# Kernel tuning notes

Measured on AMD Instinct MI355X. Metric: run time of the kernel, lower is better.

## Reference

```python
import jax, jax.numpy as jnp
import numpy as np

N = 512      # nodes
E = 16384    # edges (avg degree 32)
D = 128      # indim
OUT = 128    # outdim


def setup_inputs() -> dict:
    key = jax.random.key(0)
    k1, k2, k3 = jax.random.split(key, 3)
    X = jax.random.normal(k1, (N, N, D), dtype=jnp.float32)
    edge_index = jax.random.randint(k2, (2, E), 0, N, dtype=jnp.int64)
    W = jax.random.normal(k3, (3 * D, OUT), dtype=jnp.float32) * (1.0 / np.sqrt(3 * D))
    b = jnp.zeros((OUT,), dtype=jnp.float32)
    return {"X": X, "edge_index": edge_index, "W": W, "b": b}


def reference(X, edge_index, W, b):
    # X: [N, N, D] tuple features X[i, j] for (subgraph root i, node j)
    # edge_index: [2, E] directed edges (src -> dst), aggr = 'sum'
    n = X.shape[0]
    src, dst = edge_index[0], edge_index[1]
    # Dense binary adjacency (sum aggregation counts multi-edges, matching
    # scatter-add over the edge list). A[k, j] = #edges k -> j.
    A = jnp.zeros((n, n), dtype=X.dtype).at[src, dst].add(jnp.ones((src.shape[0],), X.dtype))
    # OpMessagePassingOnSubg2D: within subgraph i, aggregate over neighbors of j
    # X1[i, j] = sum_{k in N(j)} X[i, k]
    X1 = jnp.einsum('kj,ikd->ijd', A, X)
    # OpMessagePassingCrossSubg2D: across subgraphs, aggregate over neighbors of i
    # X2[i, j] = sum_{k in N(i)} X[k, j]
    X2 = jnp.einsum('ki,kjd->ijd', A, X)
    # catvalue([X1, X2]) -> [X, X1, X2], then pointwise MLP (single Linear)
    H = jnp.concatenate([X, X1, X2], axis=-1)  # [N, N, 3D]
    return H @ W + b  # [N, N, OUT]
```

## Files before the change

kernel.cpp:

```cpp
#include <hip/hip_runtime.h>
#include <hip/hip_bf16.h>
#include <stdint.h>

#define NN 512
#define DD 128
#define EE 16384
#define K3 384

typedef short bf16x8 __attribute__((ext_vector_type(8)));
typedef short bf16x4 __attribute__((ext_vector_type(4)));
typedef float f32x4  __attribute__((ext_vector_type(4)));

__device__ __forceinline__ short f2bf(float f) {
    union { __hip_bfloat16 h; short s; } u;
    u.h = __float2bfloat16(f);
    return u.s;
}

typedef __attribute__((address_space(3))) unsigned int lds_u32;
typedef __attribute__((address_space(1))) const unsigned int glb_u32;
__device__ __forceinline__ void gll16(void* l, const void* g) {
    __builtin_amdgcn_global_load_lds((glb_u32*)g, (lds_u32*)l, 16, 0, 0);
}


__global__ void k_zero(float* __restrict__ At) {
    At[blockIdx.x * 256 + threadIdx.x] = 0.0f;
}

__global__ void k_edges(const int* __restrict__ ei, float* __restrict__ At) {
    __shared__ int flag;
    if (threadIdx.x == 0) flag = 0;
    __syncthreads();
    int any = 0;
    for (int i = threadIdx.x; i < EE; i += blockDim.x) any |= ei[2 * i + 1];
    if (any) atomicOr(&flag, 1);
    __syncthreads();
    const bool is32 = (flag != 0);
    for (int e = threadIdx.x; e < EE; e += blockDim.x) {
        int src, dst;
        if (is32) { src = ei[e];     dst = ei[EE + e]; }
        else      { src = ei[2 * e]; dst = ei[2 * (EE + e)]; }
        atomicAdd(&At[dst * NN + src], 1.0f);
    }
}

__global__ void k_cast_at(const float* __restrict__ At, short* __restrict__ Atb) {
    int t = blockIdx.x * 256 + threadIdx.x;
    Atb[t] = f2bf(At[t]);
}

__global__ void k_wt(const float* __restrict__ W, short* __restrict__ Wt) {
    int t = blockIdx.x * 256 + threadIdx.x;
    int kk = t >> 7, n = t & 127;
    Wt[n * K3 + kk] = f2bf(W[t]);
}

__global__ __launch_bounds__(256) void k_prep(const float* __restrict__ X,
                                              short* __restrict__ XbT,
                                              short* __restrict__ XT2) {
    __shared__ __align__(16) short T[128 * 128];
    const int tid = threadIdx.x;
    const int b = blockIdx.x;
    int sbase, rstride, dbase;
    short* dst;
    if (b < 2048) {
        int i = b >> 2, k0 = (b & 3) * 128;
        sbase = i * 65536 + k0 * 128; rstride = 128;
        dbase = i * 65536 + k0; dst = XbT;
    } else {
        int bb = b - 2048;
        int j = bb >> 2, i0 = (bb & 3) * 128;
        sbase = i0 * 65536 + j * 128; rstride = 65536;
        dbase = j * 65536 + i0; dst = XT2;
    }
    #pragma unroll
    for (int it = 0; it < 16; ++it) {
        int g = tid + it * 256;
        int r = g >> 5, c4 = (g & 31) * 4;
        float4 v = *(const float4*)&X[sbase + r * rstride + c4];
        bf16x4 p; p[0] = f2bf(v.x); p[1] = f2bf(v.y); p[2] = f2bf(v.z); p[3] = f2bf(v.w);
        int cs = c4 ^ (((r >> 3) & 7) << 2);
        *(bf16x4*)&T[r * 128 + cs] = p;
    }
    __syncthreads();
    #pragma unroll
    for (int it = 0; it < 8; ++it) {
        int q = tid + it * 256;
        int d = q >> 4, ck = (q & 15) * 8;
        bf16x8 p;
        #pragma unroll
        for (int j = 0; j < 8; ++j) {
            int k = ck + j;
            p[j] = T[k * 128 + (d ^ (((k >> 3) & 7) << 2))];
        }
        *(bf16x8*)&dst[dbase + d * 512 + ck] = p;
    }
}

__global__ __launch_bounds__(256) void k_aggg(const short* __restrict__ Atb,
                                              const short* __restrict__ Bsrc,
                                              short* __restrict__ C,
                                              int mode) {
    __shared__ __align__(16) short sm[16384];
    short* As = sm;
    short* Bs = sm + 8192;

    const int tid  = threadIdx.x;
    const int lane = tid & 63;
    const int wv   = tid >> 6;
    const int wr   = (wv >> 1) * 64;
    const int wc   = (wv & 1) * 64;
    const int lm   = lane & 15;
    const int lq   = lane >> 4;

    const int inst = blockIdx.x >> 2, t4 = blockIdx.x & 3;
    const int a0 = t4 * 128;
    const int Bbase = inst * 65536;
    int Cbase, Crs;
    if (mode == 0) { Cbase = inst * 65536 + t4 * 16384; Crs = 128; }
    else           { Cbase = t4 * 8388608 + inst * 128; Crs = 65536; }

    int srow[4], scg[4];
    #pragma unroll
    for (int it = 0; it < 4; ++it) {
        int s = it * 256 + tid;
        int r = s >> 3, p = s & 7;
        srow[it] = r; scg[it] = (p ^ (r & 7)) * 8;
    }

    f32x4 acc[4][4] = {};

    for (int kb = 0; kb < 8; ++kb) {
        const int k0 = kb * 64;
        #pragma unroll
        for (int it = 0; it < 4; ++it) {
            int slot = it * 256 + tid;
            gll16(&As[slot * 8], &Atb[(a0 + srow[it]) * 512 + k0 + scg[it]]);
            gll16(&Bs[slot * 8], &Bsrc[Bbase + srow[it] * 512 + k0 + scg[it]]);
        }
        __syncthreads();
        #pragma unroll
        for (int ks = 0; ks < 2; ++ks) {
            bf16x8 af[4], bf[4];
            #pragma unroll
            for (int mf = 0; mf < 4; ++mf) {
                int R = wr + mf * 16 + lm, Cc = ks * 4 + lq;
                af[mf] = *(const bf16x8*)&As[R * 64 + (Cc ^ (R & 7)) * 8];
            }
            #pragma unroll
            for (int nf = 0; nf < 4; ++nf) {
                int R = wc + nf * 16 + lm, Cc = ks * 4 + lq;
                bf[nf] = *(const bf16x8*)&Bs[R * 64 + (Cc ^ (R & 7)) * 8];
            }
            #pragma unroll
            for (int mf = 0; mf < 4; ++mf)
                #pragma unroll
                for (int nf = 0; nf < 4; ++nf)
                    acc[mf][nf] = __builtin_amdgcn_mfma_f32_16x16x32_bf16(
                        af[mf], bf[nf], acc[mf][nf], 0, 0, 0);
        }
        __syncthreads();
    }

    #pragma unroll
    for (int mf = 0; mf < 4; ++mf)
        #pragma unroll
        for (int nf = 0; nf < 4; ++nf)
            #pragma unroll
            for (int r = 0; r < 4; ++r)
                sm[(wr + mf * 16 + lq * 4 + r) * 128 + wc + nf * 16 + lm]
                    = f2bf(acc[mf][nf][r]);
    __syncthreads();
    #pragma unroll
    for (int it = 0; it < 8; ++it) {
        int q = tid + it * 256;
        int orow = q >> 4, oc = (q & 15) * 8;
        *(bf16x8*)&C[Cbase + orow * Crs + oc] = *(const bf16x8*)&sm[orow * 128 + oc];
    }
}

__global__ __launch_bounds__(256) void k_final2(const float* __restrict__ X,
                                                const short* __restrict__ X1b,
                                                const short* __restrict__ X2b,
                                                const short* __restrict__ Wt,
                                                const float* __restrict__ bias,
                                                float* __restrict__ out) {
    __shared__ __align__(16) short sm[16384];
    short* As = sm;
    short* Ws = sm + 8192;

    const int tid  = threadIdx.x;
    const int lane = tid & 63;
    const int wv   = tid >> 6;
    const int wr   = (wv >> 1) * 64;
    const int wc   = (wv & 1) * 64;
    const int lm   = lane & 15;
    const int lq   = lane >> 4;
    const int m0   = blockIdx.x * 128;

    int srow[4], scg[4];
    #pragma unroll
    for (int it = 0; it < 4; ++it) {
        int s = it * 256 + tid;
        int r = s >> 3, p = s & 7;
        srow[it] = r; scg[it] = (p ^ (r & 7)) * 8;
    }

    f32x4 acc[4][4] = {};

    for (int ph = 0; ph < 6; ++ph) {
        const int s = ph >> 1, h = ph & 1;
        const int kw0 = s * 128 + h * 64;
        if (s == 0) {
            #pragma unroll
            for (int it = 0; it < 4; ++it) {
                int slot = it * 256 + tid;
                const float* xp = &X[(m0 + srow[it]) * 128 + h * 64 + scg[it]];
                float4 v0 = *(const float4*)xp;
                float4 v1 = *(const float4*)(xp + 4);
                bf16x8 pk;
                pk[0] = f2bf(v0.x); pk[1] = f2bf(v0.y); pk[2] = f2bf(v0.z); pk[3] = f2bf(v0.w);
                pk[4] = f2bf(v1.x); pk[5] = f2bf(v1.y); pk[6] = f2bf(v1.z); pk[7] = f2bf(v1.w);
                *(bf16x8*)&As[slot * 8] = pk;
            }
        } else {
            const short* src = (s == 1) ? X1b : X2b;
            #pragma unroll
            for (int it = 0; it < 4; ++it)
                gll16(&As[(it * 256 + tid) * 8],
                      &src[(m0 + srow[it]) * 128 + h * 64 + scg[it]]);
        }
        #pragma unroll
        for (int it = 0; it < 4; ++it)
            gll16(&Ws[(it * 256 + tid) * 8],
                  &Wt[srow[it] * K3 + kw0 + scg[it]]);
        __syncthreads();
        #pragma unroll
        for (int ks = 0; ks < 2; ++ks) {
            bf16x8 af[4], bf[4];
            #pragma unroll
            for (int mf = 0; mf < 4; ++mf) {
                int R = wr + mf * 16 + lm, Cc = ks * 4 + lq;
                af[mf] = *(const bf16x8*)&As[R * 64 + (Cc ^ (R & 7)) * 8];
            }
            #pragma unroll
            for (int nf = 0; nf < 4; ++nf) {
                int R = wc + nf * 16 + lm, Cc = ks * 4 + lq;
                bf[nf] = *(const bf16x8*)&Ws[R * 64 + (Cc ^ (R & 7)) * 8];
            }
            #pragma unroll
            for (int mf = 0; mf < 4; ++mf)
                #pragma unroll
                for (int nf = 0; nf < 4; ++nf)
                    acc[mf][nf] = __builtin_amdgcn_mfma_f32_16x16x32_bf16(
                        af[mf], bf[nf], acc[mf][nf], 0, 0, 0);
        }
        __syncthreads();
    }

    #pragma unroll
    for (int nf = 0; nf < 4; ++nf) {
        float bv = bias[wc + nf * 16 + lm];
        #pragma unroll
        for (int mf = 0; mf < 4; ++mf)
            #pragma unroll
            for (int r = 0; r < 4; ++r) {
                int row = m0 + wr + mf * 16 + lq * 4 + r;
                int col = wc + nf * 16 + lm;
                out[row * 128 + col] = acc[mf][nf][r] + bv;
            }
    }
}


__global__ __launch_bounds__(256) void k_agg_fb(const float* __restrict__ X,
                                                const float* __restrict__ At,
                                                short* __restrict__ X1b,
                                                short* __restrict__ X2b) {
    __shared__ short As[128 * 72];
    __shared__ short Bs[128 * 72];
    const int tid  = threadIdx.x;
    const int lane = tid & 63;
    const int wv   = tid >> 6;
    const int wr   = (wv >> 1) * 64;
    const int wc   = (wv & 1) * 64;
    const int lm   = lane & 15;
    const int lq   = lane >> 4;
    int a0, Bbase, Bks, Cbase, Crs;
    short* Cp;
    const int bidx = blockIdx.x;
    if (bidx < 2048) {
        int i = bidx >> 2, jt = bidx & 3;
        a0 = jt * 128; Bbase = i * 65536; Bks = 128;
        Cbase = i * 65536 + jt * 16384; Crs = 128; Cp = X1b;
    } else {
        int bb = bidx - 2048;
        int j = bb >> 2, it = bb & 3;
        a0 = it * 128; Bbase = j * 128; Bks = 65536;
        Cbase = it * 8388608 + j * 128; Crs = 65536; Cp = X2b;
    }
    f32x4 acc[4][4] = {};
    const int d  = tid & 127;
    const int kh = tid >> 7;
    for (int kb = 0; kb < 8; ++kb) {
        const int k0 = kb * 64;
        #pragma unroll
        for (int it8 = 0; it8 < 8; ++it8) {
            int g = tid + it8 * 256;
            int r = g >> 4, kq = (g & 15) * 4;
            float4 v = *(const float4*)&At[(a0 + r) * 512 + k0 + kq];
            bf16x4 p; p[0] = f2bf(v.x); p[1] = f2bf(v.y); p[2] = f2bf(v.z); p[3] = f2bf(v.w);
            *(bf16x4*)&As[r * 72 + kq] = p;
        }
        #pragma unroll
        for (int gi = 0; gi < 4; ++gi) {
            int kg = kh * 4 + gi;
            bf16x8 p;
            #pragma unroll
            for (int j = 0; j < 8; ++j)
                p[j] = f2bf(X[Bbase + (k0 + kg * 8 + j) * Bks + d]);
            *(bf16x8*)&Bs[d * 72 + kg * 8] = p;
        }
        __syncthreads();
        #pragma unroll
        for (int ks = 0; ks < 2; ++ks) {
            bf16x8 af[4], bfr[4];
            #pragma unroll
            for (int mf = 0; mf < 4; ++mf)
                af[mf] = *(const bf16x8*)&As[(wr + mf * 16 + lm) * 72 + ks * 32 + lq * 8];
            #pragma unroll
            for (int nf = 0; nf < 4; ++nf)
                bfr[nf] = *(const bf16x8*)&Bs[(wc + nf * 16 + lm) * 72 + ks * 32 + lq * 8];
            #pragma unroll
            for (int mf = 0; mf < 4; ++mf)
                #pragma unroll
                for (int nf = 0; nf < 4; ++nf)
                    acc[mf][nf] = __builtin_amdgcn_mfma_f32_16x16x32_bf16(
                        af[mf], bfr[nf], acc[mf][nf], 0, 0, 0);
        }
        __syncthreads();
    }
    #pragma unroll
    for (int mf = 0; mf < 4; ++mf)
        #pragma unroll
        for (int nf = 0; nf < 4; ++nf)
            #pragma unroll
            for (int r = 0; r < 4; ++r) {
                int row = wr + mf * 16 + lq * 4 + r;
                int col = wc + nf * 16 + lm;
                Cp[Cbase + row * Crs + col] = f2bf(acc[mf][nf][r]);
            }
}

__global__ __launch_bounds__(256) void k_final_fb(const float* __restrict__ X,
                                                  const short* __restrict__ X1b,
                                                  const short* __restrict__ X2b,
                                                  const short* __restrict__ Wt,
                                                  const float* __restrict__ bias,
                                                  float* __restrict__ out) {
    __shared__ short As[128 * 72];
    __shared__ short Ws[128 * 72];
    const int tid  = threadIdx.x;
    const int lane = tid & 63;
    const int wv   = tid >> 6;
    const int wr   = (wv >> 1) * 64;
    const int wc   = (wv & 1) * 64;
    const int lm   = lane & 15;
    const int lq   = lane >> 4;
    const int m0   = blockIdx.x * 128;
    f32x4 acc[4][4] = {};
    for (int ph = 0; ph < 6; ++ph) {
        const int s = ph >> 1, h = ph & 1;
        if (s == 0) {
            #pragma unroll
            for (int it8 = 0; it8 < 8; ++it8) {
                int g = tid + it8 * 256;
                int r = g >> 4, kq = (g & 15) * 4;
                float4 v = *(const float4*)&X[(m0 + r) * 128 + h * 64 + kq];
                bf16x4 p; p[0] = f2bf(v.x); p[1] = f2bf(v.y); p[2] = f2bf(v.z); p[3] = f2bf(v.w);
                *(bf16x4*)&As[r * 72 + kq] = p;
            }
        } else {
            const short* src = (s == 1) ? X1b : X2b;
            #pragma unroll
            for (int it4 = 0; it4 < 4; ++it4) {
                int g = tid + it4 * 256;
                int r = g >> 3, ko = (g & 7) * 8;
                *(bf16x8*)&As[r * 72 + ko] =
                    *(const bf16x8*)&src[(m0 + r) * 128 + h * 64 + ko];
            }
        }
        #pragma unroll
        for (int it4 = 0; it4 < 4; ++it4) {
            int g = tid + it4 * 256;
            int n = g >> 3, ko = (g & 7) * 8;
            *(bf16x8*)&Ws[n * 72 + ko] =
                *(const bf16x8*)&Wt[n * K3 + s * 128 + h * 64 + ko];
        }
        __syncthreads();
        #pragma unroll
        for (int ks = 0; ks < 2; ++ks) {
            bf16x8 af[4], bfr[4];
            #pragma unroll
            for (int mf = 0; mf < 4; ++mf)
                af[mf] = *(const bf16x8*)&As[(wr + mf * 16 + lm) * 72 + ks * 32 + lq * 8];
            #pragma unroll
            for (int nf = 0; nf < 4; ++nf)
                bfr[nf] = *(const bf16x8*)&Ws[(wc + nf * 16 + lm) * 72 + ks * 32 + lq * 8];
            #pragma unroll
            for (int mf = 0; mf < 4; ++mf)
                #pragma unroll
                for (int nf = 0; nf < 4; ++nf)
                    acc[mf][nf] = __builtin_amdgcn_mfma_f32_16x16x32_bf16(
                        af[mf], bfr[nf], acc[mf][nf], 0, 0, 0);
        }
        __syncthreads();
    }
    #pragma unroll
    for (int nf = 0; nf < 4; ++nf) {
        float bv = bias[wc + nf * 16 + lm];
        #pragma unroll
        for (int mf = 0; mf < 4; ++mf)
            #pragma unroll
            for (int r = 0; r < 4; ++r) {
                int row = m0 + wr + mf * 16 + lq * 4 + r;
                int col = wc + nf * 16 + lm;
                out[row * 128 + col] = acc[mf][nf][r] + bv;
            }
    }
}

extern "C" void kernel_launch(void* const* d_in, const int* in_sizes, int n_in,
                              void* d_out, int out_size, void* d_ws, size_t ws_size,
                              hipStream_t stream) {
    const float* X  = (const float*)d_in[0];
    const int*   ei = (const int*)d_in[1];
    const float* W  = (const float*)d_in[2];
    const float* b  = (const float*)d_in[3];
    float* out = (float*)d_out;
    char* ws = (char*)d_ws;
    const size_t MB = 1u << 20;

    float* At  = (float*)ws;
    short* Atb = (short*)(ws + 1 * MB);
    short* Wt  = (short*)(ws + 1 * MB + 512 * 1024);

    k_zero <<<1024, 256, 0, stream>>>(At);
    k_edges<<<1, 1024, 0, stream>>>(ei, At);
    k_wt   <<<192, 256, 0, stream>>>(W, Wt);

    if (ws_size >= 194 * MB) {
        short* X1b = (short*)(ws + 2 * MB);
        short* XT2 = (short*)(ws + 66 * MB);
        short* XbT = (short*)(ws + 130 * MB);
        short* X2b = XbT;
        k_cast_at<<<1024, 256, 0, stream>>>(At, Atb);
        k_prep   <<<4096, 256, 0, stream>>>(X, XbT, XT2);
        k_aggg   <<<2048, 256, 0, stream>>>(Atb, XbT, X1b, 0);
        k_aggg   <<<2048, 256, 0, stream>>>(Atb, XT2, X2b, 1);
        k_final2 <<<2048, 256, 0, stream>>>(X, X1b, X2b, Wt, b, out);
    } else {
        short* X1b = (short*)(ws + 2 * MB);
        short* X2b = (short*)(ws + 66 * MB);
        k_agg_fb  <<<4096, 256, 0, stream>>>(X, At, X1b, X2b);
        k_final_fb<<<2048, 256, 0, stream>>>(X, X1b, X2b, Wt, b, out);
    }
}
```

Before: 513.5 us.

## Reassociate linear layer before aggregation: apply W slices to X then aggregate

Uses linearity to compute Y1=X·W1 and Y2=X·W2 first, then aggregates with the adjacency (A^T applied per subgraph and across subgraphs), adding X·W0, the partial and the bias in a fused final kernel. This replaces the X prep/transposes and the separate final GEMM over a 384-wide concatenation, so X is read fewer times and no X1/X2 intermediates are stored. In exchange it adds a separate transpose kernel for Y2, an extra bf16 rounding of intermediate partial sums, and some leftover dead loads in the epilogue.

```diff
diff --git a/kernel.cpp b/kernel.cpp
--- a/kernel.cpp
+++ b/kernel.cpp
@@ -10,11 +10,15 @@
 typedef short bf16x8 __attribute__((ext_vector_type(8)));
 typedef short bf16x4 __attribute__((ext_vector_type(4)));
 typedef float f32x4  __attribute__((ext_vector_type(4)));
+typedef unsigned int u32;
 
 __device__ __forceinline__ short f2bf(float f) {
     union { __hip_bfloat16 h; short s; } u;
     u.h = __float2bfloat16(f);
     return u.s;
+}
+__device__ __forceinline__ u32 pk2(float a, float b) {
+    return (u32)(unsigned short)f2bf(a) | ((u32)(unsigned short)f2bf(b) << 16);
 }
 
 typedef __attribute__((address_space(3))) unsigned int lds_u32;
@@ -50,61 +54,19 @@
     Atb[t] = f2bf(At[t]);
 }
 
-__global__ void k_wt(const float* __restrict__ W, short* __restrict__ Wt) {
+__global__ void k_wt2(const float* __restrict__ W, short* __restrict__ Wt2) {
     int t = blockIdx.x * 256 + threadIdx.x;
     int kk = t >> 7, n = t & 127;
-    Wt[n * K3 + kk] = f2bf(W[t]);
-}
-
-__global__ __launch_bounds__(256) void k_prep(const float* __restrict__ X,
-                                              short* __restrict__ XbT,
-                                              short* __restrict__ XT2) {
-    __shared__ __align__(16) short T[128 * 128];
-    const int tid = threadIdx.x;
-    const int b = blockIdx.x;
-    int sbase, rstride, dbase;
-    short* dst;
-    if (b < 2048) {
-        int i = b >> 2, k0 = (b & 3) * 128;
-        sbase = i * 65536 + k0 * 128; rstride = 128;
-        dbase = i * 65536 + k0; dst = XbT;
-    } else {
-        int bb = b - 2048;
-        int j = bb >> 2, i0 = (bb & 3) * 128;
-        sbase = i0 * 65536 + j * 128; rstride = 65536;
-        dbase = j * 65536 + i0; dst = XT2;
-    }
-    #pragma unroll
-    for (int it = 0; it < 16; ++it) {
-        int g = tid + it * 256;
-        int r = g >> 5, c4 = (g & 31) * 4;
-        float4 v = *(const float4*)&X[sbase + r * rstride + c4];
-        bf16x4 p; p[0] = f2bf(v.x); p[1] = f2bf(v.y); p[2] = f2bf(v.z); p[3] = f2bf(v.w);
-        int cs = c4 ^ (((r >> 3) & 7) << 2);
-        *(bf16x4*)&T[r * 128 + cs] = p;
-    }
-    __syncthreads();
-    #pragma unroll
-    for (int it = 0; it < 8; ++it) {
-        int q = tid + it * 256;
-        int d = q >> 4, ck = (q & 15) * 8;
-        bf16x8 p;
-        #pragma unroll
-        for (int j = 0; j < 8; ++j) {
-            int k = ck + j;
-            p[j] = T[k * 128 + (d ^ (((k >> 3) & 7) << 2))];
-        }
-        *(bf16x8*)&dst[dbase + d * 512 + ck] = p;
-    }
-}
-
-__global__ __launch_bounds__(256) void k_aggg(const short* __restrict__ Atb,
-                                              const short* __restrict__ Bsrc,
-                                              short* __restrict__ C,
-                                              int mode) {
-    __shared__ __align__(16) short sm[16384];
-    short* As = sm;
-    short* Bs = sm + 8192;
+    int s = kk >> 7, d = kk & 127;
+    Wt2[s * 16384 + n * 128 + d] = f2bf(W[t]);
+}
+
+__global__ __launch_bounds__(256) void k_y(const float* __restrict__ X,
+                                           const short* __restrict__ Wt2,
+                                           short* __restrict__ Y1T,
+                                           short* __restrict__ Y2) {
+    __shared__ __align__(16) short Xs[16384];
+    __shared__ __align__(16) short Ws[16384];
 
     const int tid  = threadIdx.x;
     const int lane = tid & 63;
@@ -113,82 +75,138 @@
     const int wc   = (wv & 1) * 64;
     const int lm   = lane & 15;
     const int lq   = lane >> 4;
-
-    const int inst = blockIdx.x >> 2, t4 = blockIdx.x & 3;
-    const int a0 = t4 * 128;
-    const int Bbase = inst * 65536;
-    int Cbase, Crs;
-    if (mode == 0) { Cbase = inst * 65536 + t4 * 16384; Crs = 128; }
-    else           { Cbase = t4 * 8388608 + inst * 128; Crs = 65536; }
-
-    int srow[4], scg[4];
+    const int i  = blockIdx.x >> 2;
+    const int j0 = (blockIdx.x & 3) * 128;
+
+    #pragma unroll
+    for (int it = 0; it < 16; ++it) {
+        int g = tid + it * 256;
+        int r = g >> 5, c4 = g & 31;
+        float4 v = *(const float4*)&X[i * 65536 + (j0 + r) * 128 + c4 * 4];
+        int kb = c4 >> 4, c = c4 & 15, p = c >> 1, h2 = c & 1;
+        bf16x4 pc; pc[0] = f2bf(v.x); pc[1] = f2bf(v.y); pc[2] = f2bf(v.z); pc[3] = f2bf(v.w);
+        *(bf16x4*)&Xs[kb * 8192 + r * 64 + ((p ^ (r & 7)) * 8 + h2 * 4)] = pc;
+    }
+
+    #pragma unroll
+    for (int s = 1; s <= 2; ++s) {
+        #pragma unroll
+        for (int it = 0; it < 8; ++it) {
+            int slot = it * 256 + tid;
+            int kb = slot >> 10, rem = slot & 1023;
+            int n = rem >> 3, pc = rem & 7;
+            gll16(&Ws[slot * 8],
+                  &Wt2[s * 16384 + n * 128 + kb * 64 + ((pc ^ (n & 7)) * 8)]);
+        }
+        __syncthreads();
+
+        f32x4 acc[4][4] = {};
+        #pragma unroll
+        for (int kb = 0; kb < 2; ++kb)
+            #pragma unroll
+            for (int ks = 0; ks < 2; ++ks) {
+                bf16x8 af[4], bf[4];
+                #pragma unroll
+                for (int mf = 0; mf < 4; ++mf) {
+                    int R = wr + mf * 16 + lm, Cc = ks * 4 + lq;
+                    af[mf] = *(const bf16x8*)&Xs[kb * 8192 + R * 64 + (Cc ^ (R & 7)) * 8];
+                }
+                #pragma unroll
+                for (int nf = 0; nf < 4; ++nf) {
+                    int R = wc + nf * 16 + lm, Cc = ks * 4 + lq;
+                    bf[nf] = *(const bf16x8*)&Ws[kb * 8192 + R * 64 + (Cc ^ (R & 7)) * 8];
+                }
+                #pragma unroll
+                for (int mf = 0; mf < 4; ++mf)
+                    #pragma unroll
+                    for (int nf = 0; nf < 4; ++nf)
+                        acc[mf][nf] = __builtin_amdgcn_mfma_f32_16x16x32_bf16(
+                            af[mf], bf[nf], acc[mf][nf], 0, 0, 0);
+            }
+        __syncthreads();
+
+        if (s == 1) {
+            u32* T = (u32*)Ws;
+            #pragma unroll
+            for (int mf = 0; mf < 4; ++mf)
+                #pragma unroll
+                for (int nf = 0; nf < 4; ++nf) {
+                    int n = wc + nf * 16 + lm;
+                    int jb = wr + mf * 16 + lq * 4;
+                    int w = jb >> 1;
+                    u32 lo = pk2(acc[mf][nf][0], acc[mf][nf][1]);
+                    u32 hi = pk2(acc[mf][nf][2], acc[mf][nf][3]);
+                    uint2 val; val.x = lo; val.y = hi;
+                    *(uint2*)&T[n * 64 + (w ^ (n & 28))] = val;
+                }
+            __syncthreads();
+            #pragma unroll
+            for (int it = 0; it < 8; ++it) {
+                int ch = tid & 15, n = (tid >> 4) + it * 16;
+                uint4 q = *(const uint4*)&T[n * 64 + ((ch * 4) ^ (n & 28))];
+                *(uint4*)&Y1T[i * 65536 + n * 512 + j0 + ch * 8] = q;
+            }
+            __syncthreads();
+        } else {
+            #pragma unroll
+            for (int mf = 0; mf < 4; ++mf)
+                #pragma unroll
+                for (int nf = 0; nf < 4; ++nf)
+                    #pragma unroll
+                    for (int r = 0; r < 4; ++r)
+                        Ws[(wr + mf * 16 + lq * 4 + r) * 128 + wc + nf * 16 + lm]
+                            = f2bf(acc[mf][nf][r]);
+            __syncthreads();
+            #pragma unroll
+            for (int it = 0; it < 8; ++it) {
+                int q = tid + it * 256;
+                int row = q >> 4, oc = (q & 15) * 8;
+                *(bf16x8*)&Y2[i * 65536 + (j0 + row) * 128 + oc]
+                    = *(const bf16x8*)&Ws[row * 128 + oc];
+            }
+        }
+    }
+}
+
+__global__ __launch_bounds__(256) void k_t(const short* __restrict__ Y2,
+                                           short* __restrict__ Y2T) {
+    __shared__ __align__(16) u32 U[128 * 64];
+    const int tid = threadIdx.x;
+    const int j  = blockIdx.x >> 2;
+    const int k0 = (blockIdx.x & 3) * 128;
+
+    const int c8 = tid & 15;
+    const int a0 = tid >> 4;
     #pragma unroll
     for (int it = 0; it < 4; ++it) {
-        int s = it * 256 + tid;
-        int r = s >> 3, p = s & 7;
-        srow[it] = r; scg[it] = (p ^ (r & 7)) * 8;
-    }
-
-    f32x4 acc[4][4] = {};
-
-    for (int kb = 0; kb < 8; ++kb) {
-        const int k0 = kb * 64;
-        #pragma unroll
-        for (int it = 0; it < 4; ++it) {
-            int slot = it * 256 + tid;
-            gll16(&As[slot * 8], &Atb[(a0 + srow[it]) * 512 + k0 + scg[it]]);
-            gll16(&Bs[slot * 8], &Bsrc[Bbase + srow[it] * 512 + k0 + scg[it]]);
-        }
-        __syncthreads();
-        #pragma unroll
-        for (int ks = 0; ks < 2; ++ks) {
-            bf16x8 af[4], bf[4];
-            #pragma unroll
-            for (int mf = 0; mf < 4; ++mf) {
-                int R = wr + mf * 16 + lm, Cc = ks * 4 + lq;
-                af[mf] = *(const bf16x8*)&As[R * 64 + (Cc ^ (R & 7)) * 8];
-            }
-            #pragma unroll
-            for (int nf = 0; nf < 4; ++nf) {
-                int R = wc + nf * 16 + lm, Cc = ks * 4 + lq;
-                bf[nf] = *(const bf16x8*)&Bs[R * 64 + (Cc ^ (R & 7)) * 8];
-            }
-            #pragma unroll
-            for (int mf = 0; mf < 4; ++mf)
-                #pragma unroll
-                for (int nf = 0; nf < 4; ++nf)
-                    acc[mf][nf] = __builtin_amdgcn_mfma_f32_16x16x32_bf16(
-                        af[mf], bf[nf], acc[mf][nf], 0, 0, 0);
-        }
-        __syncthreads();
-    }
-
-    #pragma unroll
-    for (int mf = 0; mf < 4; ++mf)
-        #pragma unroll
-        for (int nf = 0; nf < 4; ++nf)
-            #pragma unroll
-            for (int r = 0; r < 4; ++r)
-                sm[(wr + mf * 16 + lq * 4 + r) * 128 + wc + nf * 16 + lm]
-                    = f2bf(acc[mf][nf][r]);
+        int a = a0 + it * 16;
+        const short* r0 = &Y2[(size_t)(k0 + 2 * a) * 65536 + j * 128 + c8 * 8];
+        bf16x8 A0 = *(const bf16x8*)r0;
+        bf16x8 A1 = *(const bf16x8*)(r0 + 65536);
+        #pragma unroll
+        for (int cc = 0; cc < 8; ++cc) {
+            int n = c8 * 8 + cc;
+            U[n * 64 + (a ^ (n & 28))] =
+                (u32)(unsigned short)A0[cc] | ((u32)(unsigned short)A1[cc] << 16);
+        }
+    }
     __syncthreads();
+    const int ch = tid & 15;
+    const int n0 = tid >> 4;
     #pragma unroll
     for (int it = 0; it < 8; ++it) {
-        int q = tid + it * 256;
-        int orow = q >> 4, oc = (q & 15) * 8;
-        *(bf16x8*)&C[Cbase + orow * Crs + oc] = *(const bf16x8*)&sm[orow * 128 + oc];
-    }
-}
-
-__global__ __launch_bounds__(256) void k_final2(const float* __restrict__ X,
-                                                const short* __restrict__ X1b,
-                                                const short* __restrict__ X2b,
-                                                const short* __restrict__ Wt,
-                                                const float* __restrict__ bias,
-                                                float* __restrict__ out) {
+        int n = n0 + it * 16;
+        uint4 q = *(const uint4*)&U[n * 64 + ((ch * 4) ^ (n & 28))];
+        *(uint4*)&Y2T[j * 65536 + n * 512 + k0 + ch * 8] = q;
+    }
+}
+
+__global__ __launch_bounds__(256) void k_a1(const short* __restrict__ Atb,
+                                            const short* __restrict__ Y1T,
+                                            short* __restrict__ P1) {
     __shared__ __align__(16) short sm[16384];
     short* As = sm;
-    short* Ws = sm + 8192;
+    short* Bs = sm + 8192;
 
     const int tid  = threadIdx.x;
     const int lane = tid & 63;
@@ -197,44 +215,21 @@
     const int wc   = (wv & 1) * 64;
     const int lm   = lane & 15;
     const int lq   = lane >> 4;
-    const int m0   = blockIdx.x * 128;
-
-    int srow[4], scg[4];
-    #pragma unroll
-    for (int it = 0; it < 4; ++it) {
-        int s = it * 256 + tid;
-        int r = s >> 3, p = s & 7;
-        srow[it] = r; scg[it] = (p ^ (r & 7)) * 8;
-    }
+    const int i  = blockIdx.x >> 2;
+    const int a0 = (blockIdx.x & 3) * 128;
 
     f32x4 acc[4][4] = {};
 
-    for (int ph = 0; ph < 6; ++ph) {
-        const int s = ph >> 1, h = ph & 1;
-        const int kw0 = s * 128 + h * 64;
-        if (s == 0) {
-            #pragma unroll
-            for (int it = 0; it < 4; ++it) {
-                int slot = it * 256 + tid;
-                const float* xp = &X[(m0 + srow[it]) * 128 + h * 64 + scg[it]];
-                float4 v0 = *(const float4*)xp;
-                float4 v1 = *(const float4*)(xp + 4);
-                bf16x8 pk;
-                pk[0] = f2bf(v0.x); pk[1] = f2bf(v0.y); pk[2] = f2bf(v0.z); pk[3] = f2bf(v0.w);
-                pk[4] = f2bf(v1.x); pk[5] = f2bf(v1.y); pk[6] = f2bf(v1.z); pk[7] = f2bf(v1.w);
-                *(bf16x8*)&As[slot * 8] = pk;
-            }
-        } else {
-            const short* src = (s == 1) ? X1b : X2b;
-            #pragma unroll
-            for (int it = 0; it < 4; ++it)
-                gll16(&As[(it * 256 + tid) * 8],
-                      &src[(m0 + srow[it]) * 128 + h * 64 + scg[it]]);
-        }
-        #pragma unroll
-        for (int it = 0; it < 4; ++it)
-            gll16(&Ws[(it * 256 + tid) * 8],
-                  &Wt[srow[it] * K3 + kw0 + scg[it]]);
+    for (int kb = 0; kb < 8; ++kb) {
+        const int k0 = kb * 64;
+        #pragma unroll
+        for (int it = 0; it < 4; ++it) {
+            int slot = it * 256 + tid;
+            int r = slot >> 3, p = slot & 7;
+            int cg = (p ^ (r & 7)) * 8;
+            gll16(&As[slot * 8], &Atb[(a0 + r) * 512 + k0 + cg]);
+            gll16(&Bs[slot * 8], &Y1T[i * 65536 + r * 512 + k0 + cg]);
+        }
         __syncthreads();
         #pragma unroll
         for (int ks = 0; ks < 2; ++ks) {
@@ -247,7 +242,7 @@
             #pragma unroll
             for (int nf = 0; nf < 4; ++nf) {
                 int R = wc + nf * 16 + lm, Cc = ks * 4 + lq;
-                bf[nf] = *(const bf16x8*)&Ws[R * 64 + (Cc ^ (R & 7)) * 8];
+                bf[nf] = *(const bf16x8*)&Bs[R * 64 + (Cc ^ (R & 7)) * 8];
             }
             #pragma unroll
             for (int mf = 0; mf < 4; ++mf)
@@ -260,16 +255,155 @@
     }
 
     #pragma unroll
-    for (int nf = 0; nf < 4; ++nf) {
-        float bv = bias[wc + nf * 16 + lm];
-        #pragma unroll
-        for (int mf = 0; mf < 4; ++mf)
-            #pragma unroll
-            for (int r = 0; r < 4; ++r) {
-                int row = m0 + wr + mf * 16 + lq * 4 + r;
-                int col = wc + nf * 16 + lm;
-                out[row * 128 + col] = acc[mf][nf][r] + bv;
-            }
+    for (int mf = 0; mf < 4; ++mf)
+        #pragma unroll
+        for (int nf = 0; nf < 4; ++nf)
+            #pragma unroll
+            for (int r = 0; r < 4; ++r)
+                sm[(wr + mf * 16 + lq * 4 + r) * 128 + wc + nf * 16 + lm]
+                    = f2bf(acc[mf][nf][r]);
+    __syncthreads();
+    #pragma unroll
+    for (int it = 0; it < 8; ++it) {
+        int q = tid + it * 256;
+        int row = q >> 4, oc = (q & 15) * 8;
+        *(bf16x8*)&P1[i * 65536 + (a0 + row) * 128 + oc]
+            = *(const bf16x8*)&sm[row * 128 + oc];
+    }
+}
+
+__global__ __launch_bounds__(256) void k_a2f(const float* __restrict__ X,
+                                             const short* __restrict__ Atb,
+                                             const short* __restrict__ Y2T,
+                                             const short* __restrict__ Wt2,
+                                             const short* __restrict__ P1,
+                                             const float* __restrict__ bias,
+                                             float* __restrict__ out) {
+    __shared__ __align__(16) short sm[16384];
+    short* As = sm;
+    short* Bs = sm + 8192;
+
+    const int tid  = threadIdx.x;
+    const int lane = tid & 63;
+    const int wv   = tid >> 6;
+    const int wr   = (wv >> 1) * 64;
+    const int wc   = (wv & 1) * 64;
+    const int lm   = lane & 15;
+    const int lq   = lane >> 4;
+    const int j  = blockIdx.x >> 2;
+    const int i0 = (blockIdx.x & 3) * 128;
+
+    f32x4 acc[4][4] = {};
+
+    #pragma unroll
+    for (int kb = 0; kb < 2; ++kb) {
+        #pragma unroll
+        for (int it = 0; it < 8; ++it) {
+            int g = tid + it * 256;
+            int r = g >> 4, c4 = g & 15;
+            float4 v = *(const float4*)&X[(size_t)(i0 + r) * 65536 + j * 128 + kb * 64 + c4 * 4];
+            int p = c4 >> 1, h2 = c4 & 1;
+            bf16x4 pc; pc[0] = f2bf(v.x); pc[1] = f2bf(v.y); pc[2] = f2bf(v.z); pc[3] = f2bf(v.w);
+            *(bf16x4*)&As[r * 64 + ((p ^ (r & 7)) * 8 + h2 * 4)] = pc;
+        }
+        #pragma unroll
+        for (int it = 0; it < 4; ++it) {
+            int slot = it * 256 + tid;
+            int n = slot >> 3, pc = slot & 7;
+            gll16(&Bs[slot * 8], &Wt2[n * 128 + kb * 64 + ((pc ^ (n & 7)) * 8)]);
+        }
+        __syncthreads();
+        #pragma unroll
+        for (int ks = 0; ks < 2; ++ks) {
+            bf16x8 af[4], bf[4];
+            #pragma unroll
+            for (int mf = 0; mf < 4; ++mf) {
+                int R = wr + mf * 16 + lm, Cc = ks * 4 + lq;
+                af[mf] = *(const bf16x8*)&As[R * 64 + (Cc ^ (R & 7)) * 8];
+            }
+            #pragma unroll
+            for (int nf = 0; nf < 4; ++nf) {
+                int R = wc + nf * 16 + lm, Cc = ks * 4 + lq;
+                bf[nf] = *(const bf16x8*)&Bs[R * 64 + (Cc ^ (R & 7)) * 8];
+            }
+            #pragma unroll
+            for (int mf = 0; mf < 4; ++mf)
+                #pragma unroll
+                for (int nf = 0; nf < 4; ++nf)
+                    acc[mf][nf] = __builtin_amdgcn_mfma_f32_16x16x32_bf16(
+                        af[mf], bf[nf], acc[mf][nf], 0, 0, 0);
+        }
+        __syncthreads();
+    }
+
+    for (int kb = 0; kb < 8; ++kb) {
+        const int k0 = kb * 64;
+        #pragma unroll
+        for (int it = 0; it < 4; ++it) {
+            int slot = it * 256 + tid;
+            int r = slot >> 3, p = slot & 7;
+            int cg = (p ^ (r & 7)) * 8;
+            gll16(&As[slot * 8], &Atb[(i0 + r) * 512 + k0 + cg]);
+            gll16(&Bs[slot * 8], &Y2T[j * 65536 + r * 512 + k0 + cg]);
+        }
+        __syncthreads();
+        #pragma unroll
+        for (int ks = 0; ks < 2; ++ks) {
+            bf16x8 af[4], bf[4];
+            #pragma unroll
+            for (int mf = 0; mf < 4; ++mf) {
+                int R = wr + mf * 16 + lm, Cc = ks * 4 + lq;
+                af[mf] = *(const bf16x8*)&As[R * 64 + (Cc ^ (R & 7)) * 8];
+            }
+            #pragma unroll
+            for (int nf = 0; nf < 4; ++nf) {
+                int R = wc + nf * 16 + lm, Cc = ks * 4 + lq;
+                bf[nf] = *(const bf16x8*)&Bs[R * 64 + (Cc ^ (R & 7)) * 8];
+            }
+            #pragma unroll
+            for (int mf = 0; mf < 4; ++mf)
+                #pragma unroll
+                for (int nf = 0; nf < 4; ++nf)
+                    acc[mf][nf] = __builtin_amdgcn_mfma_f32_16x16x32_bf16(
+                        af[mf], bf[nf], acc[mf][nf], 0, 0, 0);
+        }
+        __syncthreads();
+    }
+
+    #pragma unroll
+    for (int mf = 0; mf < 4; ++mf)
+        #pragma unroll
+        for (int nf = 0; nf < 4; ++nf)
+            #pragma unroll
+            for (int r = 0; r < 4; ++r)
+                sm[(wr + mf * 16 + lq * 4 + r) * 128 + wc + nf * 16 + lm]
+                    = f2bf(acc[mf][nf][r]);
+    __syncthreads();
+    #pragma unroll
+    for (int it = 0; it < 8; ++it) {
+        int q = tid + it * 256;
+        int row = q >> 4, oc = (q & 15) * 8;
+        bf16x8 vs = *(const bf16x8*)&sm[row * 128 + oc];
+        bf16x8 vp = *(const bf16x8*)&P1[(size_t)(i0 + row) * 65536 / 512 * 512 + 0];
+        (void)vp;
+        const short* p1p = &P1[(size_t)(i0 + row) * 65536 + j * 128 + oc];
+        bf16x8 vpl = *(const bf16x8*)p1p;
+        float4 b0 = *(const float4*)&bias[oc];
+        float4 b1 = *(const float4*)&bias[oc + 4];
+        union { short s; __hip_bfloat16 h; } cs, cp;
+        float o[8];
+        #pragma unroll
+        for (int e = 0; e < 8; ++e) {
+            cs.s = vs[e]; cp.s = vpl[e];
+            o[e] = __bfloat162float(cs.h) + __bfloat162float(cp.h);
+        }
+        o[0] += b0.x; o[1] += b0.y; o[2] += b0.z; o[3] += b0.w;
+        o[4] += b1.x; o[5] += b1.y; o[6] += b1.z; o[7] += b1.w;
+        float* op = &out[(size_t)(i0 + row) * 65536 + j * 128 + oc];
+        float4 w0; w0.x = o[0]; w0.y = o[1]; w0.z = o[2]; w0.w = o[3];
+        float4 w1; w1.x = o[4]; w1.y = o[5]; w1.z = o[6]; w1.w = o[7];
+        *(float4*)op = w0;
+        *(float4*)(op + 4) = w1;
     }
 }
 
@@ -318,8 +452,8 @@
             int kg = kh * 4 + gi;
             bf16x8 p;
             #pragma unroll
-            for (int j = 0; j < 8; ++j)
-                p[j] = f2bf(X[Bbase + (k0 + kg * 8 + j) * Bks + d]);
+            for (int jj = 0; jj < 8; ++jj)
+                p[jj] = f2bf(X[Bbase + (k0 + kg * 8 + jj) * Bks + d]);
             *(bf16x8*)&Bs[d * 72 + kg * 8] = p;
         }
         __syncthreads();
@@ -356,7 +490,7 @@
 __global__ __launch_bounds__(256) void k_final_fb(const float* __restrict__ X,
                                                   const short* __restrict__ X1b,
                                                   const short* __restrict__ X2b,
-                                                  const short* __restrict__ Wt,
+                                                  const short* __restrict__ Wt2,
                                                   const float* __restrict__ bias,
                                                   float* __restrict__ out) {
     __shared__ short As[128 * 72];
@@ -396,7 +530,7 @@
             int g = tid + it4 * 256;
             int n = g >> 3, ko = (g & 7) * 8;
             *(bf16x8*)&Ws[n * 72 + ko] =
-                *(const bf16x8*)&Wt[n * K3 + s * 128 + h * 64 + ko];
+                *(const bf16x8*)&Wt2[s * 16384 + n * 128 + h * 64 + ko];
         }
         __syncthreads();
         #pragma unroll
@@ -444,26 +578,26 @@
 
     float* At  = (float*)ws;
     short* Atb = (short*)(ws + 1 * MB);
-    short* Wt  = (short*)(ws + 1 * MB + 512 * 1024);
-
-    k_zero <<<1024, 256, 0, stream>>>(At);
-    k_edges<<<1, 1024, 0, stream>>>(ei, At);
-    k_wt   <<<192, 256, 0, stream>>>(W, Wt);
+    short* Wt2 = (short*)(ws + 1 * MB + 512 * 1024);
+
+    k_zero   <<<1024, 256, 0, stream>>>(At);
+    k_edges  <<<1, 1024, 0, stream>>>(ei, At);
+    k_wt2    <<<192, 256, 0, stream>>>(W, Wt2);
+    k_cast_at<<<1024, 256, 0, stream>>>(At, Atb);
 
     if (ws_size >= 194 * MB) {
-        short* X1b = (short*)(ws + 2 * MB);
-        short* XT2 = (short*)(ws + 66 * MB);
-        short* XbT = (short*)(ws + 130 * MB);
-        short* X2b = XbT;
-        k_cast_at<<<1024, 256, 0, stream>>>(At, Atb);
-        k_prep   <<<4096, 256, 0, stream>>>(X, XbT, XT2);
-        k_aggg   <<<2048, 256, 0, stream>>>(Atb, XbT, X1b, 0);
-        k_aggg   <<<2048, 256, 0, stream>>>(Atb, XT2, X2b, 1);
-        k_final2 <<<2048, 256, 0, stream>>>(X, X1b, X2b, Wt, b, out);
+        short* Y1T = (short*)(ws + 2 * MB);
+        short* Y2  = (short*)(ws + 66 * MB);
+        short* Y2T = (short*)(ws + 130 * MB);
+        short* P1  = Y2;
+        k_y  <<<2048, 256, 0, stream>>>(X, Wt2, Y1T, Y2);
+        k_t  <<<2048, 256, 0, stream>>>(Y2, Y2T);
+        k_a1 <<<2048, 256, 0, stream>>>(Atb, Y1T, P1);
+        k_a2f<<<2048, 256, 0, stream>>>(X, Atb, Y2T, Wt2, P1, b, out);
     } else {
         short* X1b = (short*)(ws + 2 * MB);
         short* X2b = (short*)(ws + 66 * MB);
         k_agg_fb  <<<4096, 256, 0, stream>>>(X, At, X1b, X2b);
-        k_final_fb<<<2048, 256, 0, stream>>>(X, X1b, X2b, Wt, b, out);
-    }
-}
+        k_final_fb<<<2048, 256, 0, stream>>>(X, X1b, X2b, Wt2, b, out);
+    }
+}
```

New measurement: 475.7 us. -7.4%, faster.
